# Kernel optimization log

Hardware: AMD Instinct MI355X
Metric: run time of the kernel (lower is better)

## Reference

```python
import jax, jax.numpy as jnp
import numpy as np

ADC_F_BITS = 4
BIT_SCALE = 0.05
# clamp upper bound: 2^(7-f) - 1/2^f
CLAMP_MAX = 2.0 ** (7 - ADC_F_BITS) - 1.0 / 2.0 ** ADC_F_BITS  # 7.9375
N_LEVELS = 127  # 7-bit ADC characteristic


def setup_inputs() -> dict:
    key = jax.random.key(0)
    kx, kc = jax.random.split(key)
    # conv-feature-map-like activations; scale so a good fraction lies in [0, CLAMP_MAX]
    x = jax.random.normal(kx, (128, 128, 56, 56), dtype=jnp.float32) * 2.0
    # monotone ADC threshold characteristic spanning the clamp range
    adc_char = jnp.sort(
        jax.random.uniform(kc, (N_LEVELS,), dtype=jnp.float32) * CLAMP_MAX
    )
    return {"x": x, "adc_char": adc_char}


def reference(x, adc_char):
    # activation = clamp(x, 0, 2^(7-f) - 1/2^f)
    a = jnp.clip(x, 0.0, CLAMP_MAX)
    # quant_op_int = sum(a[..., None] >= adc_char, axis=-1)
    # adc_char is sorted, so this equals the count of thresholds <= a,
    # i.e. searchsorted(side='right') -- avoids the [*, 127] bool intermediate.
    q = jnp.searchsorted(adc_char, a, side="right").astype(jnp.float32)
    # op = bit_scale * quant_op_int / 2^f
    return BIT_SCALE * (q / 2.0 ** ADC_F_BITS)
```

## Files before the change

kernel.cpp:

```cpp
#include <hip/hip_runtime.h>


#define N_LEVELS 127
#define CLAMP_MAX 7.9375f
#define OUT_SCALE 0.003125f

__device__ __forceinline__ float adc_one(const float* __restrict__ my, float x) {
    float a = fminf(fmaxf(x, 0.0f), CLAMP_MAX);
    int cnt = 0;
    if (my[(cnt + 63) << 5] <= a) cnt += 64;
    if (my[(cnt + 31) << 5] <= a) cnt += 32;
    if (my[(cnt + 15) << 5] <= a) cnt += 16;
    if (my[(cnt +  7) << 5] <= a) cnt += 8;
    if (my[(cnt +  3) << 5] <= a) cnt += 4;
    if (my[(cnt +  1) << 5] <= a) cnt += 2;
    if (my[(cnt +  0) << 5] <= a) cnt += 1;
    return OUT_SCALE * (float)cnt;
}

__global__ __launch_bounds__(256) void ADCActivation_55465207660703_kernel(
        const float* __restrict__ x,
        const float* __restrict__ adc_char,
        float* __restrict__ out,
        int n4, int rem) {
    __shared__ float lut[N_LEVELS * 32];

    const int tid = threadIdx.x;
    for (int i = tid; i < N_LEVELS * 32; i += 256) {
        lut[i] = adc_char[i >> 5];
    }
    __syncthreads();

    const float* my = lut + (tid & 31);

    const float4* __restrict__ x4 = (const float4*)x;
    float4* __restrict__ o4 = (float4*)out;

    int idx = blockIdx.x * 256 + tid;
    const int stride = gridDim.x * 256;
    for (int i = idx; i < n4; i += stride) {
        float4 v = x4[i];
        float4 r;
        r.x = adc_one(my, v.x);
        r.y = adc_one(my, v.y);
        r.z = adc_one(my, v.z);
        r.w = adc_one(my, v.w);
        o4[i] = r;
    }

    if (blockIdx.x == 0 && tid < rem) {
        int e = n4 * 4 + tid;
        out[e] = adc_one(my, x[e]);
    }
}

extern "C" void kernel_launch(void* const* d_in, const int* in_sizes, int n_in,
                              void* d_out, int out_size, void* d_ws, size_t ws_size,
                              hipStream_t stream) {
    const float* x        = (const float*)d_in[0];
    const float* adc_char = (const float*)d_in[1];
    float* out            = (float*)d_out;

    const int n   = in_sizes[0];
    const int n4  = n >> 2;
    const int rem = n & 3;

    int blocks = (n4 + 255) / 256;
    if (blocks > 2048) blocks = 2048;
    if (blocks < 1) blocks = 1;

    ADCActivation_55465207660703_kernel<<<blocks, 256, 0, stream>>>(x, adc_char, out, n4, rem);
}
```

Measured before the change: 83.81 us.

## Replace binary search with bucketed lookup table for ADC thresholds

Swaps the 7-step binary search over a bank-replicated threshold LUT for a 1024-bucket direct-index table. Each bucket stores the count of thresholds below it plus the first threshold inside it, so most elements need one shared-memory float2 read and one compare. Buckets holding more than one threshold fall back to a short linear scan, which causes divergence. Each thread also handles two float4s per iteration, and the table build adds per-block setup work.

```diff
diff --git a/kernel.cpp b/kernel.cpp
--- a/kernel.cpp
+++ b/kernel.cpp
@@ -1,20 +1,25 @@
 #include <hip/hip_runtime.h>
+#include <math.h>
 
 
 #define N_LEVELS 127
 #define CLAMP_MAX 7.9375f
 #define OUT_SCALE 0.003125f
+#define NBUCKETS 1024
 
-__device__ __forceinline__ float adc_one(const float* __restrict__ my, float x) {
+__device__ __forceinline__ float adc_eval(const float2* __restrict__ table,
+                                          const float* __restrict__ th,
+                                          float x) {
     float a = fminf(fmaxf(x, 0.0f), CLAMP_MAX);
-    int cnt = 0;
-    if (my[(cnt + 63) << 5] <= a) cnt += 64;
-    if (my[(cnt + 31) << 5] <= a) cnt += 32;
-    if (my[(cnt + 15) << 5] <= a) cnt += 16;
-    if (my[(cnt +  7) << 5] <= a) cnt += 8;
-    if (my[(cnt +  3) << 5] <= a) cnt += 4;
-    if (my[(cnt +  1) << 5] <= a) cnt += 2;
-    if (my[(cnt +  0) << 5] <= a) cnt += 1;
+    int idx = (int)(a * 128.0f);
+    float2 e = table[idx];
+    int meta = __float_as_int(e.x);
+    int lo = meta & 0xFF;
+    int hi = meta >> 8;
+    int cnt = lo + (e.y <= a ? 1 : 0);
+    if (hi > lo + 1) {
+        for (int j = lo + 1; j < hi; ++j) cnt += (th[j] <= a ? 1 : 0);
+    }
     return OUT_SCALE * (float)cnt;
 }
 
@@ -23,34 +28,65 @@
         const float* __restrict__ adc_char,
         float* __restrict__ out,
         int n4, int rem) {
-    __shared__ float lut[N_LEVELS * 32];
+    __shared__ float  th[128];
+    __shared__ int    bk[128];
+    __shared__ float2 table[NBUCKETS];
 
     const int tid = threadIdx.x;
-    for (int i = tid; i < N_LEVELS * 32; i += 256) {
-        lut[i] = adc_char[i >> 5];
+
+    if (tid < N_LEVELS) {
+        float t = adc_char[tid];
+        th[tid] = t;
+        bk[tid] = (int)(t * 128.0f);
+    }
+    if (tid == N_LEVELS) th[tid] = INFINITY;
+    __syncthreads();
+
+    {
+        const int b0 = tid, b1 = tid + 256, b2 = tid + 512, b3 = tid + 768;
+        int lo0 = 0, hi0 = 0, lo1 = 0, hi1 = 0, lo2 = 0, hi2 = 0, lo3 = 0, hi3 = 0;
+        for (int j = 0; j < N_LEVELS; ++j) {
+            int bj = bk[j];
+            lo0 += (bj < b0); hi0 += (bj <= b0);
+            lo1 += (bj < b1); hi1 += (bj <= b1);
+            lo2 += (bj < b2); hi2 += (bj <= b2);
+            lo3 += (bj < b3); hi3 += (bj <= b3);
+        }
+        table[b0] = make_float2(__int_as_float(lo0 | (hi0 << 8)), th[lo0 < hi0 ? lo0 : 127]);
+        table[b1] = make_float2(__int_as_float(lo1 | (hi1 << 8)), th[lo1 < hi1 ? lo1 : 127]);
+        table[b2] = make_float2(__int_as_float(lo2 | (hi2 << 8)), th[lo2 < hi2 ? lo2 : 127]);
+        table[b3] = make_float2(__int_as_float(lo3 | (hi3 << 8)), th[lo3 < hi3 ? lo3 : 127]);
     }
     __syncthreads();
-
-    const float* my = lut + (tid & 31);
 
     const float4* __restrict__ x4 = (const float4*)x;
     float4* __restrict__ o4 = (float4*)out;
 
-    int idx = blockIdx.x * 256 + tid;
-    const int stride = gridDim.x * 256;
-    for (int i = idx; i < n4; i += stride) {
-        float4 v = x4[i];
-        float4 r;
-        r.x = adc_one(my, v.x);
-        r.y = adc_one(my, v.y);
-        r.z = adc_one(my, v.z);
-        r.w = adc_one(my, v.w);
-        o4[i] = r;
+    const int stride = gridDim.x * 512;
+    for (int i0 = blockIdx.x * 512 + tid; i0 < n4; i0 += stride) {
+        const int i1 = i0 + 256;
+        const bool p1 = i1 < n4;
+        float4 v0 = x4[i0];
+        float4 v1 = make_float4(0.f, 0.f, 0.f, 0.f);
+        if (p1) v1 = x4[i1];
+
+        float4 r0, r1;
+        r0.x = adc_eval(table, th, v0.x);
+        r0.y = adc_eval(table, th, v0.y);
+        r0.z = adc_eval(table, th, v0.z);
+        r0.w = adc_eval(table, th, v0.w);
+        r1.x = adc_eval(table, th, v1.x);
+        r1.y = adc_eval(table, th, v1.y);
+        r1.z = adc_eval(table, th, v1.z);
+        r1.w = adc_eval(table, th, v1.w);
+
+        o4[i0] = r0;
+        if (p1) o4[i1] = r1;
     }
 
     if (blockIdx.x == 0 && tid < rem) {
         int e = n4 * 4 + tid;
-        out[e] = adc_one(my, x[e]);
+        out[e] = adc_eval(table, th, x[e]);
     }
 }
 
@@ -65,7 +101,7 @@
     const int n4  = n >> 2;
     const int rem = n & 3;
 
-    int blocks = (n4 + 255) / 256;
+    int blocks = (n4 + 511) / 512;
     if (blocks > 2048) blocks = 2048;
     if (blocks < 1) blocks = 1;
 
```

Measured after the change: 93.71 us. 1.12x slower.

## Replace per-element binary search with bucketed threshold lookup table

Applied to the files above, without the earlier changes.

Adds a one-block build kernel that buckets the ADC thresholds into 1024 uniform bins, each storing a base count and up to three in-bin thresholds. The main kernel then does one shared-memory float4 lookup plus three compares per element instead of a 7-step dependent binary search. It falls back to a linear scan if any bucket has more than three thresholds. It also processes four float4 per thread per iteration with a fixed grid, at the cost of an extra kernel launch and a workspace dependency.

```diff
diff --git a/kernel.cpp b/kernel.cpp
--- a/kernel.cpp
+++ b/kernel.cpp
@@ -1,11 +1,123 @@
 #include <hip/hip_runtime.h>
+#include <math.h>
 
 
 #define N_LEVELS 127
 #define CLAMP_MAX 7.9375f
 #define OUT_SCALE 0.003125f
+#define NBUCKETS 1024
 
-__device__ __forceinline__ float adc_one(const float* __restrict__ my, float x) {
+__global__ __launch_bounds__(256) void adc_build_kernel(
+        const float* __restrict__ adc_char,
+        float4* __restrict__ tbl,
+        float* __restrict__ th_g,
+        int* __restrict__ deep_g) {
+    __shared__ float th[128];
+    __shared__ int   bk[128];
+    __shared__ int   deep_s;
+    const int tid = threadIdx.x;
+    if (tid == 0) deep_s = 0;
+    if (tid < N_LEVELS) {
+        float t = adc_char[tid];
+        th[tid] = t;
+        bk[tid] = (int)(t * 128.0f);
+    }
+    if (tid == N_LEVELS) th[tid] = INFINITY;
+    __syncthreads();
+    #pragma unroll
+    for (int q = 0; q < 4; ++q) {
+        const int b = tid + q * 256;
+        int lo = 0, hi = 0;
+        for (int j = 0; j < N_LEVELS; ++j) {
+            int bj = bk[j];
+            lo += (bj < b);
+            hi += (bj <= b);
+        }
+        int i0 = (lo + 0 < hi) ? lo + 0 : 127;
+        int i1 = (lo + 1 < hi) ? lo + 1 : 127;
+        int i2 = (lo + 2 < hi) ? lo + 2 : 127;
+        tbl[b] = make_float4(__int_as_float(lo), th[i0], th[i1], th[i2]);
+        if (hi - lo > 3) atomicOr(&deep_s, 1);
+    }
+    if (tid < 128) th_g[tid] = th[tid];
+    __syncthreads();
+    if (tid == 0) deep_g[0] = deep_s;
+}
+
+__device__ __forceinline__ float adc_fast(const float4* __restrict__ lt, float x) {
+    float a = fminf(fmaxf(x, 0.0f), CLAMP_MAX);
+    int idx = (int)(a * 128.0f);
+    float4 e = lt[idx];
+    int cnt = __float_as_int(e.x);
+    cnt += (e.y <= a);
+    cnt += (e.z <= a);
+    cnt += (e.w <= a);
+    return OUT_SCALE * (float)cnt;
+}
+
+__global__ __launch_bounds__(256) void adc_main_kernel(
+        const float* __restrict__ x,
+        float* __restrict__ out,
+        const float4* __restrict__ tbl,
+        const float* __restrict__ th_g,
+        const int* __restrict__ deep_g,
+        int K) {
+    __shared__ float4 lt[NBUCKETS];
+    __shared__ float  th[128];
+    const int tid = threadIdx.x;
+    #pragma unroll
+    for (int j = 0; j < 4; ++j)
+        lt[j * 256 + tid] = tbl[j * 256 + tid];
+    const int deep = __builtin_amdgcn_readfirstlane(deep_g[0]);
+    if (deep && tid < 128) th[tid] = th_g[tid];
+    __syncthreads();
+
+    const float4* __restrict__ x4 = (const float4*)x;
+    float4* __restrict__ o4 = (float4*)out;
+
+    if (!deep) {
+        for (int k = 0; k < K; ++k) {
+            const int base = (k * gridDim.x + blockIdx.x) * 1024 + tid;
+            float4 v0 = x4[base];
+            float4 v1 = x4[base + 256];
+            float4 v2 = x4[base + 512];
+            float4 v3 = x4[base + 768];
+            float4 r0, r1, r2, r3;
+            r0.x = adc_fast(lt, v0.x); r0.y = adc_fast(lt, v0.y);
+            r0.z = adc_fast(lt, v0.z); r0.w = adc_fast(lt, v0.w);
+            r1.x = adc_fast(lt, v1.x); r1.y = adc_fast(lt, v1.y);
+            r1.z = adc_fast(lt, v1.z); r1.w = adc_fast(lt, v1.w);
+            r2.x = adc_fast(lt, v2.x); r2.y = adc_fast(lt, v2.y);
+            r2.z = adc_fast(lt, v2.z); r2.w = adc_fast(lt, v2.w);
+            r3.x = adc_fast(lt, v3.x); r3.y = adc_fast(lt, v3.y);
+            r3.z = adc_fast(lt, v3.z); r3.w = adc_fast(lt, v3.w);
+            o4[base]       = r0;
+            o4[base + 256] = r1;
+            o4[base + 512] = r2;
+            o4[base + 768] = r3;
+        }
+    } else {
+        for (int k = 0; k < K; ++k) {
+            const int base = (k * gridDim.x + blockIdx.x) * 1024 + tid;
+            #pragma unroll
+            for (int j = 0; j < 4; ++j) {
+                float4 v = x4[base + j * 256];
+                float4 r;
+                float* vp = (float*)&v; float* rp = (float*)&r;
+                #pragma unroll
+                for (int c = 0; c < 4; ++c) {
+                    float a = fminf(fmaxf(vp[c], 0.0f), CLAMP_MAX);
+                    int cnt = 0;
+                    for (int t = 0; t < N_LEVELS; ++t) cnt += (th[t] <= a);
+                    rp[c] = OUT_SCALE * (float)cnt;
+                }
+                o4[base + j * 256] = r;
+            }
+        }
+    }
+}
+
+__device__ __forceinline__ float adc_bs(const float* __restrict__ my, float x) {
     float a = fminf(fmaxf(x, 0.0f), CLAMP_MAX);
     int cnt = 0;
     if (my[(cnt + 63) << 5] <= a) cnt += 64;
@@ -18,39 +130,29 @@
     return OUT_SCALE * (float)cnt;
 }
 
-__global__ __launch_bounds__(256) void ADCActivation_55465207660703_kernel(
+__global__ __launch_bounds__(256) void adc_generic_kernel(
         const float* __restrict__ x,
         const float* __restrict__ adc_char,
         float* __restrict__ out,
         int n4, int rem) {
     __shared__ float lut[N_LEVELS * 32];
-
     const int tid = threadIdx.x;
-    for (int i = tid; i < N_LEVELS * 32; i += 256) {
-        lut[i] = adc_char[i >> 5];
-    }
+    for (int i = tid; i < N_LEVELS * 32; i += 256) lut[i] = adc_char[i >> 5];
     __syncthreads();
-
     const float* my = lut + (tid & 31);
-
     const float4* __restrict__ x4 = (const float4*)x;
     float4* __restrict__ o4 = (float4*)out;
-
-    int idx = blockIdx.x * 256 + tid;
     const int stride = gridDim.x * 256;
-    for (int i = idx; i < n4; i += stride) {
+    for (int i = blockIdx.x * 256 + tid; i < n4; i += stride) {
         float4 v = x4[i];
         float4 r;
-        r.x = adc_one(my, v.x);
-        r.y = adc_one(my, v.y);
-        r.z = adc_one(my, v.z);
-        r.w = adc_one(my, v.w);
+        r.x = adc_bs(my, v.x); r.y = adc_bs(my, v.y);
+        r.z = adc_bs(my, v.z); r.w = adc_bs(my, v.w);
         o4[i] = r;
     }
-
     if (blockIdx.x == 0 && tid < rem) {
         int e = n4 * 4 + tid;
-        out[e] = adc_one(my, x[e]);
+        out[e] = adc_bs(my, x[e]);
     }
 }
 
@@ -61,13 +163,31 @@
     const float* adc_char = (const float*)d_in[1];
     float* out            = (float*)d_out;
 
-    const int n   = in_sizes[0];
-    const int n4  = n >> 2;
-    const int rem = n & 3;
+    const int n  = in_sizes[0];
+    const int n4 = n >> 2;
 
-    int blocks = (n4 + 255) / 256;
-    if (blocks > 2048) blocks = 2048;
-    if (blocks < 1) blocks = 1;
+    const size_t WS_NEED = 16384 + 512 + 4;
+    bool ws_ok = (ws_size >= WS_NEED) && ((n & 3) == 0);
 
-    ADCActivation_55465207660703_kernel<<<blocks, 256, 0, stream>>>(x, adc_char, out, n4, rem);
+    int blocks = 0, K = 0;
+    if (ws_ok && (n4 % 1024) == 0) {
+        int chunks = n4 / 1024;
+        if (chunks % 1792 == 0)      { blocks = 1792;   K = chunks / 1792; }
+        else if (chunks <= 4096)     { blocks = chunks; K = 1; }
+    }
+
+    if (blocks > 0) {
+        char* ws = (char*)d_ws;
+        float4* tbl  = (float4*)ws;
+        float*  th_g = (float*)(ws + 16384);
+        int*    deep = (int*)(ws + 16896);
+        adc_build_kernel<<<1, 256, 0, stream>>>(adc_char, tbl, th_g, deep);
+        adc_main_kernel<<<blocks, 256, 0, stream>>>(x, out, tbl, th_g, deep, K);
+    } else {
+        int rem = n & 3;
+        int gb = (n4 + 255) / 256;
+        if (gb > 2048) gb = 2048;
+        if (gb < 1) gb = 1;
+        adc_generic_kernel<<<gb, 256, 0, stream>>>(x, adc_char, out, n4, rem);
+    }
 }
```

After: 96.13 us. +14.7%, slower.

## Resolve top search levels with register selects and process two float4 per thread

Applied to the files above, without the earlier changes.

Replaces the first four levels of the shared-memory binary search with thresholds held in registers, chosen by branch-free selects, so only the last three levels read the LDS lookup table. Each thread also loads and processes two float4 vectors per loop iteration, which raises memory-level parallelism, and the grid size is adjusted to match. This removes four dependent LDS loads per element in exchange for extra VALU select instructions and higher register pressure.

```diff
diff --git a/kernel.cpp b/kernel.cpp
--- a/kernel.cpp
+++ b/kernel.cpp
@@ -1,20 +1,43 @@
 #include <hip/hip_runtime.h>
+#include <math.h>
 
 
 #define N_LEVELS 127
 #define CLAMP_MAX 7.9375f
 #define OUT_SCALE 0.003125f
 
-__device__ __forceinline__ float adc_one(const float* __restrict__ my, float x) {
+struct TreeT {
+    float T63;
+    float T31, T95;
+    float T15, T47, T79, T111;
+    float Q0, Q1, Q2, Q3, Q4, Q5, Q6, Q7;
+};
+
+__device__ __forceinline__ float adc_eval(const float* __restrict__ my,
+                                          const TreeT& t, float x) {
     float a = fminf(fmaxf(x, 0.0f), CLAMP_MAX);
-    int cnt = 0;
-    if (my[(cnt + 63) << 5] <= a) cnt += 64;
-    if (my[(cnt + 31) << 5] <= a) cnt += 32;
-    if (my[(cnt + 15) << 5] <= a) cnt += 16;
-    if (my[(cnt +  7) << 5] <= a) cnt += 8;
-    if (my[(cnt +  3) << 5] <= a) cnt += 4;
-    if (my[(cnt +  1) << 5] <= a) cnt += 2;
-    if (my[(cnt +  0) << 5] <= a) cnt += 1;
+
+    bool m0 = (t.T63 <= a);
+    float s1 = m0 ? t.T95 : t.T31;
+    bool m1 = (s1 <= a);
+    float u0 = m0 ? t.T79  : t.T15;
+    float u1 = m0 ? t.T111 : t.T47;
+    float s2 = m1 ? u1 : u0;
+    bool m2 = (s2 <= a);
+    float x0 = m2 ? t.Q1 : t.Q0;
+    float x1 = m2 ? t.Q3 : t.Q2;
+    float x2 = m2 ? t.Q5 : t.Q4;
+    float x3 = m2 ? t.Q7 : t.Q6;
+    float y0 = m1 ? x1 : x0;
+    float y1 = m1 ? x3 : x2;
+    float s3 = m0 ? y1 : y0;
+    bool m3 = (s3 <= a);
+    int cnt = (m0 ? 64 : 0) + (m1 ? 32 : 0) + (m2 ? 16 : 0) + (m3 ? 8 : 0);
+
+    if (my[(cnt + 3) << 5] <= a) cnt += 4;
+    if (my[(cnt + 1) << 5] <= a) cnt += 2;
+    if (my[(cnt + 0) << 5] <= a) cnt += 1;
+
     return OUT_SCALE * (float)cnt;
 }
 
@@ -26,31 +49,49 @@
     __shared__ float lut[N_LEVELS * 32];
 
     const int tid = threadIdx.x;
-    for (int i = tid; i < N_LEVELS * 32; i += 256) {
-        lut[i] = adc_char[i >> 5];
-    }
+    for (int i = tid; i < N_LEVELS * 32; i += 256) lut[i] = adc_char[i >> 5];
     __syncthreads();
+
+    TreeT t;
+    t.T63 = adc_char[63];
+    t.T31 = adc_char[31];  t.T95  = adc_char[95];
+    t.T15 = adc_char[15];  t.T47  = adc_char[47];
+    t.T79 = adc_char[79];  t.T111 = adc_char[111];
+    t.Q0 = adc_char[7];    t.Q1 = adc_char[23];
+    t.Q2 = adc_char[39];   t.Q3 = adc_char[55];
+    t.Q4 = adc_char[71];   t.Q5 = adc_char[87];
+    t.Q6 = adc_char[103];  t.Q7 = adc_char[119];
 
     const float* my = lut + (tid & 31);
 
     const float4* __restrict__ x4 = (const float4*)x;
     float4* __restrict__ o4 = (float4*)out;
 
-    int idx = blockIdx.x * 256 + tid;
-    const int stride = gridDim.x * 256;
-    for (int i = idx; i < n4; i += stride) {
-        float4 v = x4[i];
-        float4 r;
-        r.x = adc_one(my, v.x);
-        r.y = adc_one(my, v.y);
-        r.z = adc_one(my, v.z);
-        r.w = adc_one(my, v.w);
-        o4[i] = r;
+    const int stride = gridDim.x * 512;
+    for (int i0 = blockIdx.x * 512 + tid; i0 < n4; i0 += stride) {
+        const int i1 = i0 + 256;
+        const bool p1 = i1 < n4;
+        float4 v0 = x4[i0];
+        float4 v1 = make_float4(0.f, 0.f, 0.f, 0.f);
+        if (p1) v1 = x4[i1];
+
+        float4 r0, r1;
+        r0.x = adc_eval(my, t, v0.x);
+        r0.y = adc_eval(my, t, v0.y);
+        r0.z = adc_eval(my, t, v0.z);
+        r0.w = adc_eval(my, t, v0.w);
+        r1.x = adc_eval(my, t, v1.x);
+        r1.y = adc_eval(my, t, v1.y);
+        r1.z = adc_eval(my, t, v1.z);
+        r1.w = adc_eval(my, t, v1.w);
+
+        o4[i0] = r0;
+        if (p1) o4[i1] = r1;
     }
 
     if (blockIdx.x == 0 && tid < rem) {
         int e = n4 * 4 + tid;
-        out[e] = adc_one(my, x[e]);
+        out[e] = adc_eval(my, t, x[e]);
     }
 }
 
@@ -65,7 +106,7 @@
     const int n4  = n >> 2;
     const int rem = n & 3;
 
-    int blocks = (n4 + 255) / 256;
+    int blocks = (n4 + 511) / 512;
     if (blocks > 2048) blocks = 2048;
     if (blocks < 1) blocks = 1;
 
```

Result: slower. 86.04 us (+2.7%).
